# Performance work log

Measured on AMD Instinct MI355X. Metric: run time of the kernel, lower is better.

## Reference

```python
import jax, jax.numpy as jnp
import numpy as np

B, N, OBS_DIM = 64, 512, 128
HIDDEN_DIM, MESSAGE_DIM, ACTION_DIM = 256, 128, 16


def _dense_params(key, din, dout):
    kw, kb = jax.random.split(key)
    W = jax.random.normal(kw, (din, dout), jnp.float32) * 0.02
    b = jnp.zeros((dout,), jnp.float32)
    return W, b


def setup_inputs() -> dict:
    key = jax.random.key(0)
    ks = jax.random.split(key, 12)
    obs_batch = jax.random.normal(ks[0], (B, N, OBS_DIM), jnp.float32)
    dones_batch = jnp.zeros((B, N), jnp.bool_)
    We, be = _dense_params(ks[1], OBS_DIM, HIDDEN_DIM)
    Wc, bc = _dense_params(ks[2], HIDDEN_DIM, MESSAGE_DIM // 4)
    Wn, bn = _dense_params(ks[3], HIDDEN_DIM, MESSAGE_DIM // 2)
    Wb, bb = _dense_params(ks[4], HIDDEN_DIM, MESSAGE_DIM // 4)
    Wi, bi = _dense_params(ks[5], HIDDEN_DIM, 1)
    Wq, bq = _dense_params(ks[6], HIDDEN_DIM, MESSAGE_DIM)
    Wk, bk = _dense_params(ks[7], MESSAGE_DIM, MESSAGE_DIM)
    Wv, bv = _dense_params(ks[8], MESSAGE_DIM, MESSAGE_DIM)
    Wp, bp = _dense_params(ks[9], HIDDEN_DIM + MESSAGE_DIM, HIDDEN_DIM)
    Wa, ba = _dense_params(ks[10], HIDDEN_DIM, ACTION_DIM)
    Wcr, bcr = _dense_params(ks[11], HIDDEN_DIM, 1)
    return {"obs_batch": obs_batch, "dones_batch": dones_batch,
            "We": We, "be": be, "Wc": Wc, "bc": bc, "Wn": Wn, "bn": bn,
            "Wb": Wb, "bb": bb, "Wi": Wi, "bi": bi, "Wq": Wq, "bq": bq,
            "Wk": Wk, "bk": bk, "Wv": Wv, "bv": bv, "Wp": Wp, "bp": bp,
            "Wa": Wa, "ba": ba, "Wcr": Wcr, "bcr": bcr}


def reference(obs_batch, dones_batch, We, be, Wc, bc, Wn, bn, Wb, bb, Wi, bi,
              Wq, bq, Wk, bk, Wv, bv, Wp, bp, Wa, ba, Wcr, bcr):
    dense = lambda x, W, b: x @ W + b
    encoded = jax.nn.relu(dense(obs_batch, We, be))                 # [B,N,H]
    messages = jnp.concatenate([dense(encoded, Wc, bc),
                                dense(encoded, Wn, bn),
                                dense(encoded, Wb, bb)], axis=-1)   # [B,N,M]
    importance = jax.nn.sigmoid(dense(encoded, Wi, bi))             # [B,N,1]
    Q = dense(encoded, Wq, bq)
    K = dense(messages, Wk, bk)
    V = dense(messages, Wv, bv)
    scores = jnp.einsum('bqd,bkd->bqk', Q, K) / jnp.sqrt(jnp.float32(MESSAGE_DIM))
    importance_weights = importance * jnp.transpose(importance, (0, 2, 1))  # [B,N,N]
    scores = scores * importance_weights
    norms = jnp.linalg.norm(obs_batch, axis=-1, keepdims=True)      # [B,N,1]
    obs_sim = jnp.einsum('bid,bjd->bij', obs_batch, obs_batch)
    obs_sim = obs_sim / (norms + 1e-08)
    obs_sim = obs_sim / (jnp.transpose(norms, (0, 2, 1)) + 1e-08)
    scores = scores + obs_sim * 0.5
    attn = jax.nn.softmax(scores, axis=-1)
    aggregated = jnp.einsum('bqk,bkd->bqd', attn, V)                # [B,N,M]
    combined = jnp.concatenate([encoded, aggregated], axis=-1)
    x = jax.nn.relu(dense(combined, Wp, bp))
    logits = dense(x, Wa, ba)
    value = dense(x, Wcr, bcr).squeeze(-1)
    return (logits, value)
```

## Files before the change

### kernel.cpp

```cpp
#include <hip/hip_runtime.h>
#include <math.h>


typedef __attribute__((ext_vector_type(8))) short short8;
typedef __attribute__((ext_vector_type(4))) float f32x4;

#define RSQRT_D 0.08838834764831843f
#define MFMA __builtin_amdgcn_mfma_f32_16x16x32_bf16

__device__ __forceinline__ unsigned short f2bf(float f) {
  union { float f; unsigned u; } v; v.f = f;
  return (unsigned short)((v.u + 0x7FFFu + ((v.u >> 16) & 1u)) >> 16);
}
__device__ __forceinline__ float bf2f(unsigned short h) {
  union { unsigned u; float f; } v; v.u = ((unsigned)h) << 16;
  return v.f;
}
__device__ __forceinline__ unsigned pack2(float a, float b) {
  return (unsigned)f2bf(a) | ((unsigned)f2bf(b) << 16);
}
__device__ __forceinline__ short8 ld8(const unsigned short* p) {
  return *(const short8*)p;
}
__device__ __forceinline__ void gl16(const unsigned short* g,
                                     unsigned short* l) {
  __builtin_amdgcn_global_load_lds(
      (const __attribute__((address_space(1))) unsigned int*)(const void*)g,
      (__attribute__((address_space(3))) unsigned int*)(void*)l, 16, 0, 0);
}

__global__ __launch_bounds__(256) void prep_all(
    const float* __restrict__ obs, const float* __restrict__ We,
    const float* __restrict__ Wq, const float* __restrict__ Wk,
    const float* __restrict__ Wv, const float* __restrict__ Wp,
    const float* __restrict__ Wc, const float* __restrict__ Wn,
    const float* __restrict__ Wb, const float* __restrict__ bc,
    const float* __restrict__ bn, const float* __restrict__ bb,
    const float* __restrict__ Wa, const float* __restrict__ Wcr,
    const float* __restrict__ ba, const float* __restrict__ bcr,
    const float* __restrict__ bq, const float* __restrict__ bk,
    const float* __restrict__ bv, unsigned short* __restrict__ WeT,
    unsigned short* __restrict__ Wqkv, unsigned short* __restrict__ WpT,
    unsigned short* __restrict__ WaCrT, float* __restrict__ bqkv,
    unsigned short* __restrict__ obs_bf, unsigned short* __restrict__ As,
    unsigned short* __restrict__ Bs, float* __restrict__ logits,
    float* __restrict__ value) {
  const int bid = blockIdx.x, tid = threadIdx.x;
  if (bid < 673) {
    int idx = bid * 256 + tid;
    if (idx < 32768) {
      int n = idx >> 7, k = idx & 127;
      WeT[idx] = f2bf(We[k * 256 + n]);
    } else if (idx < 65536) {
      int i = idx - 32768;
      int n = i >> 8, k = i & 255;
      Wqkv[i] = f2bf(Wq[k * 128 + n]);
    } else if (idx < 163840) {
      int i = idx - 65536;
      int n = i / 384, k = i - n * 384;
      WpT[i] = f2bf(Wp[k * 256 + n]);
    } else if (idx < 172032) {
      int i = idx - 163840;
      int n = i >> 8, k = i & 255;
      float v = (n < 16) ? Wa[k * 16 + n] : (n == 16) ? Wcr[k] : 0.f;
      WaCrT[i] = f2bf(v);
    } else if (idx < 172160) {
      int i = idx - 172032;
      bqkv[i] = bq[i];
    }
  } else if (bid < 2721) {
    const int wave = tid >> 6, lane = tid & 63;
    const int t0 = (bid - 673) * 16 + wave * 4;
#pragma unroll
    for (int it = 0; it < 4; ++it) {
      int t = t0 + it;
      const float* row = obs + (size_t)t * 128;
      float2 o = *(const float2*)(row + lane * 2);
      float s2 = o.x * o.x + o.y * o.y;
#pragma unroll
      for (int off = 1; off < 64; off <<= 1) s2 += __shfl_xor(s2, off);
      float inv = 1.f / (sqrtf(s2) + 1e-8f);
      ((unsigned*)obs_bf)[(size_t)t * 64 + lane] = pack2(o.x, o.y);
      ((unsigned*)As)[(size_t)t * 128 + 64 + lane] =
          pack2(o.x * 0.5f * inv, o.y * 0.5f * inv);
      ((unsigned*)Bs)[(size_t)t * 128 + 64 + lane] =
          pack2(o.x * inv, o.y * inv);
    }
  } else if (bid < 4897) {
    int i = (bid - 2721) * 256 + tid;
    if (i < 524288) logits[i] = ba[i & 15];
    else value[i - 524288] = bcr[0];
  } else if (bid < 4905) {
    const int wb = bid - 4897;
    const int lane = tid & 63, wave = tid >> 6;
    const int quad = lane >> 4, l16 = lane & 15;
    const int r0 = wb * 32;
    f32x4 acc[2][4];
#pragma unroll
    for (int i = 0; i < 2; ++i)
#pragma unroll
      for (int j = 0; j < 4; ++j) acc[i][j] = (f32x4){0.f, 0.f, 0.f, 0.f};
#pragma unroll
    for (int kc = 0; kc < 4; ++kc) {
      short8 af[2], bf[4];
#pragma unroll
      for (int i = 0; i < 2; ++i) {
        int n = r0 + i * 16 + l16;
        const float* src = (n < 128) ? (Wk + n) : (Wv + (n - 128));
        short8 v;
#pragma unroll
        for (int e = 0; e < 8; ++e)
          v[e] = (short)f2bf(src[(size_t)(kc * 32 + quad * 8 + e) * 128]);
        af[i] = v;
      }
#pragma unroll
      for (int j = 0; j < 4; ++j) {
        int h = wave * 64 + j * 16 + l16;
        int m0 = kc * 32 + quad * 8;
        const float* p = (m0 < 32)   ? (Wc + (size_t)h * 32 + m0)
                       : (m0 < 96)   ? (Wn + (size_t)h * 64 + (m0 - 32))
                                     : (Wb + (size_t)h * 32 + (m0 - 96));
        short8 v;
#pragma unroll
        for (int e = 0; e < 8; ++e) v[e] = (short)f2bf(p[e]);
        bf[j] = v;
      }
#pragma unroll
      for (int i = 0; i < 2; ++i)
#pragma unroll
        for (int j = 0; j < 4; ++j)
          acc[i][j] = MFMA(af[i], bf[j], acc[i][j], 0, 0, 0);
    }
#pragma unroll
    for (int i = 0; i < 2; ++i) {
      const int row = r0 + i * 16 + quad * 4;
#pragma unroll
      for (int j = 0; j < 4; ++j) {
        const int col = wave * 64 + j * 16 + l16;
#pragma unroll
        for (int r = 0; r < 4; ++r)
          Wqkv[(size_t)(128 + row + r) * 256 + col] = f2bf(acc[i][j][r]);
      }
    }
  } else {
    int i = tid;
    float acc = (i < 128) ? bk[i] : bv[i - 128];
    for (int m = 0; m < 128; ++m) {
      float bmv = (m < 32) ? bc[m] : (m < 96) ? bn[m - 32] : bb[m - 96];
      float w = (i < 128) ? Wk[(size_t)m * 128 + i]
                          : Wv[(size_t)m * 128 + (i - 128)];
      acc += bmv * bf2f(f2bf(w));
    }
    bqkv[128 + i] = acc;
  }
}

__global__ __launch_bounds__(256, 2) void encqkv(
    const unsigned short* __restrict__ obs_bf,
    const unsigned short* __restrict__ WeT, const float* __restrict__ be,
    const float* __restrict__ Wi, const float* __restrict__ bi,
    const unsigned short* __restrict__ Wqkv, const float* __restrict__ bqkv,
    unsigned short* __restrict__ enc, unsigned short* __restrict__ As,
    unsigned short* __restrict__ Bs, unsigned short* __restrict__ vT) {
  __shared__ char smem[81920];
  unsigned short* Asr = (unsigned short*)smem;
  unsigned short* Bsr = (unsigned short*)(smem + 16384);
  unsigned short* encl = (unsigned short*)smem;
  unsigned short* Bq = (unsigned short*)(smem + 32768);
  float* imp_lds = (float*)(smem + 65536);
  const int tid = threadIdx.x, lane = tid & 63, wave = tid >> 6;
  const int quad = lane >> 4, l16 = lane & 15;
  const int bm0 = blockIdx.x * 64;

#pragma unroll
  for (int it = 0; it < 4; ++it) {
    int c = it * 256 + tid;
    int row = c >> 4, ch = c & 15;
    gl16(obs_bf + (size_t)(bm0 + row) * 128 + ((ch ^ (row & 15)) << 3),
         Asr + it * 2048 + wave * 512);
  }
#pragma unroll
  for (int it = 0; it < 16; ++it) {
    int c = it * 256 + tid;
    int row = c >> 4, ch = c & 15;
    gl16(WeT + (size_t)row * 128 + ((ch ^ (row & 15)) << 3),
         Bsr + it * 2048 + wave * 512);
  }
  __syncthreads();

  f32x4 acc[4][4];
#pragma unroll
  for (int i = 0; i < 4; ++i)
#pragma unroll
    for (int j = 0; j < 4; ++j) acc[i][j] = (f32x4){0.f, 0.f, 0.f, 0.f};
#pragma unroll
  for (int ks = 0; ks < 4; ++ks) {
    short8 af[4], bf[4];
#pragma unroll
    for (int mi = 0; mi < 4; ++mi) {
      int row = mi * 16 + l16;
      af[mi] = *(const short8*)&Asr[row * 128 + (((ks * 4 + quad) ^ (row & 15)) << 3)];
    }
#pragma unroll
    for (int ni = 0; ni < 4; ++ni) {
      int row = wave * 64 + ni * 16 + l16;
      bf[ni] = *(const short8*)&Bsr[row * 128 + (((ks * 4 + quad) ^ (row & 15)) << 3)];
    }
#pragma unroll
    for (int mi = 0; mi < 4; ++mi)
#pragma unroll
      for (int ni = 0; ni < 4; ++ni)
        acc[mi][ni] = MFMA(af[mi], bf[ni], acc[mi][ni], 0, 0, 0);
  }
  __syncthreads();

  if (tid < 64) imp_lds[tid] = 0.f;
  __syncthreads();

  {
#pragma unroll
    for (int i = 0; i < 4; ++i) {
      int row = i * 32 + (tid >> 3);
      gl16(Wqkv + (size_t)row * 256 + (((tid & 7) ^ (row & 7)) << 3),
           Bq + i * 2048 + wave * 512);
    }
  }

  const float bi0 = bi[0];
#pragma unroll
  for (int mi = 0; mi < 4; ++mi) {
    const int rowl = mi * 16 + quad * 4;
    float ip[4] = {0.f, 0.f, 0.f, 0.f};
#pragma unroll
    for (int ni = 0; ni < 4; ++ni) {
      const int col = wave * 64 + ni * 16 + l16;
      const float bvv = be[col], wv = Wi[col];
      const int kh = col >> 7, ic = col & 127;
#pragma unroll
      for (int r = 0; r < 4; ++r) {
        const int row = rowl + r;
        float v = fmaxf(acc[mi][ni][r] + bvv, 0.f);
        enc[(size_t)(bm0 + row) * 256 + col] = f2bf(v);
        encl[kh * 8192 + row * 128 + (((ic >> 3) ^ (row & 15)) << 3) + (ic & 7)] =
            f2bf(v);
        ip[r] += v * wv;
      }
    }
#pragma unroll
    for (int r = 0; r < 4; ++r) {
#pragma unroll
      for (int off = 1; off < 16; off <<= 1) ip[r] += __shfl_xor(ip[r], off);
    }
    if (l16 == 0) {
#pragma unroll
      for (int r = 0; r < 4; ++r) atomicAdd(&imp_lds[rowl + r], ip[r]);
    }
  }
  __syncthreads();

  const int wm = wave & 1, wn = wave >> 1;
  for (int ct = 0; ct < 3; ++ct) {
    f32x4 a2[2][4];
#pragma unroll
    for (int i = 0; i < 2; ++i)
#pragma unroll
      for (int j = 0; j < 4; ++j) a2[i][j] = (f32x4){0.f, 0.f, 0.f, 0.f};
#pragma unroll
    for (int kt = 0; kt < 4; ++kt) {
      if (kt < 3 || ct < 2) {
        const int nct = (kt < 3) ? ct : ct + 1;
        const int nkt = (kt < 3) ? kt + 1 : 0;
        const int nbo = ((kt + 1) & 1) * 8192;
#pragma unroll
        for (int i = 0; i < 4; ++i) {
          int row = i * 32 + (tid >> 3);
          gl16(Wqkv + (size_t)(nct * 128 + row) * 256 + nkt * 64 +
                   (((tid & 7) ^ (row & 7)) << 3),
               Bq + nbo + i * 2048 + wave * 512);
        }
      }
      const int bo = (kt & 1) * 8192;
#pragma unroll
      for (int ks2 = 0; ks2 < 2; ++ks2) {
        const int kc = kt * 2 + ks2;
        const int kh = kc >> 2, c4 = kc & 3;
        short8 af2[2], bf2[4];
#pragma unroll
        for (int mi = 0; mi < 2; ++mi) {
          int row = wm * 32 + mi * 16 + l16;
          af2[mi] = *(const short8*)&encl[kh * 8192 + row * 128 +
                                          (((c4 * 4 + quad) ^ (row & 15)) << 3)];
        }
#pragma unroll
        for (int ni = 0; ni < 4; ++ni) {
          int row = wn * 64 + ni * 16 + l16;
          bf2[ni] = *(const short8*)&Bq[bo + row * 64 +
                                        (((ks2 * 4 + quad) ^ (row & 7)) << 3)];
        }
#pragma unroll
        for (int mi = 0; mi < 2; ++mi)
#pragma unroll
          for (int ni = 0; ni < 4; ++ni)
            a2[mi][ni] = MFMA(af2[mi], bf2[ni], a2[mi][ni], 0, 0, 0);
      }
      __syncthreads();
    }

#pragma unroll
    for (int mi = 0; mi < 2; ++mi) {
      const int rowl = wm * 32 + mi * 16 + quad * 4;
      const int rowb = bm0 + rowl;
      float sg[4];
      if (ct < 2) {
        const float mult = (ct == 0) ? RSQRT_D : 1.0f;
#pragma unroll
        for (int r = 0; r < 4; ++r)
          sg[r] = mult / (1.f + __expf(-(imp_lds[rowl + r] + bi0)));
      }
#pragma unroll
      for (int ni = 0; ni < 4; ++ni) {
        const int col = wn * 64 + ni * 16 + l16;
        const float bvv = bqkv[ct * 128 + col];
        if (ct == 0) {
#pragma unroll
          for (int r = 0; r < 4; ++r)
            As[(size_t)(rowb + r) * 256 + col] =
                f2bf((a2[mi][ni][r] + bvv) * sg[r]);
        } else if (ct == 1) {
#pragma unroll
          for (int r = 0; r < 4; ++r)
            Bs[(size_t)(rowb + r) * 256 + col] =
                f2bf((a2[mi][ni][r] + bvv) * sg[r]);
        } else {
          uint2 o;
          o.x = pack2(a2[mi][ni][0] + bvv, a2[mi][ni][1] + bvv);
          o.y = pack2(a2[mi][ni][2] + bvv, a2[mi][ni][3] + bvv);
          *(uint2*)(vT + ((size_t)(rowb >> 9) * 128 + col) * 512 +
                    (rowb & 511)) = o;
        }
      }
    }
  }
}

__global__ __launch_bounds__(512, 4) void flash4b(
    const unsigned short* __restrict__ As, const unsigned short* __restrict__ Bs,
    const unsigned short* __restrict__ vT, unsigned short* __restrict__ agg) {
  __shared__ unsigned short Ub[16384];
  __shared__ unsigned short Pp[8192];
  __shared__ float redm[2][64];
  __shared__ float reds[2][64];
  const int tid = threadIdx.x, lane = tid & 63, wave = tid >> 6;
  const int quad = lane >> 4, l16 = lane & 15;
  const int wm = wave & 3, wn = wave >> 2;
  const int b = blockIdx.x & 63;
  const int qt = blockIdx.x >> 6;
  const size_t tok0 = (size_t)b * 512 + qt * 64;
  const int srow = tid >> 4, slc = tid & 15;
  const int qr8 = tid >> 3, ql8 = tid & 7;

  short8 af[8];
#pragma unroll
  for (int kc = 0; kc < 8; ++kc)
    af[kc] = ld8(As + (tok0 + wm * 16 + l16) * 256 + kc * 32 + quad * 8);

  f32x4 s[4][4];
#pragma unroll
  for (int kt = 0; kt < 4; ++kt)
#pragma unroll
    for (int nt = 0; nt < 4; ++nt) s[kt][nt] = (f32x4){0.f, 0.f, 0.f, 0.f};

  auto qstage = [&](int c) {
    const int kt_ = c >> 2, dq_ = c & 3;
#pragma unroll
    for (int r2 = 0; r2 < 2; ++r2) {
      int row = r2 * 64 + qr8;
      gl16(Bs + ((size_t)b * 512 + kt_ * 128 + row) * 256 + dq_ * 64 +
               ((ql8 ^ (row & 7)) << 3),
           Ub + (c & 1) * 8192 + r2 * 4096 + wave * 512);
    }
  };
  qstage(0);
  __syncthreads();
#pragma unroll 16
  for (int c = 0; c < 16; ++c) {
    if (c < 15) qstage(c + 1);
    const int kt = c >> 2, dq = c & 3;
    const int ub0 = (c & 1) * 8192;
#pragma unroll
    for (int kk2 = 0; kk2 < 2; ++kk2) {
      short8 bfr[4];
#pragma unroll
      for (int nt = 0; nt < 4; ++nt) {
        int rr = wn * 64 + nt * 16 + l16;
        bfr[nt] = *(const short8*)&Ub[ub0 + rr * 64 +
                                      (((kk2 * 2 + quad) ^ (rr & 7)) << 3)];
      }
#pragma unroll
      for (int nt = 0; nt < 4; ++nt)
        s[kt][nt] = MFMA(af[dq * 2 + kk2], bfr[nt], s[kt][nt], 0, 0, 0);
    }
    __syncthreads();
  }

  const int rbase = wm * 16 + quad * 4;
  float mt[4];
#pragma unroll
  for (int r = 0; r < 4; ++r) {
    float mv = -1e30f;
#pragma unroll
    for (int kt = 0; kt < 4; ++kt)
#pragma unroll
      for (int nt = 0; nt < 4; ++nt) mv = fmaxf(mv, s[kt][nt][r]);
#pragma unroll
    for (int off = 1; off < 16; off <<= 1) mv = fmaxf(mv, __shfl_xor(mv, off));
    mt[r] = mv;
  }
  if (l16 == 0) {
#pragma unroll
    for (int r = 0; r < 4; ++r) redm[wn][rbase + r] = mt[r];
  }
  __syncthreads();
  float lsum[4];
#pragma unroll
  for (int r = 0; r < 4; ++r) {
    float mfull = fmaxf(mt[r], redm[1 ^ wn][rbase + r]);
    float sum = 0.f;
#pragma unroll
    for (int kt = 0; kt < 4; ++kt)
#pragma unroll
      for (int nt = 0; nt < 4; ++nt) {
        float p = __expf(s[kt][nt][r] - mfull);
        s[kt][nt][r] = p;
        sum += p;
      }
#pragma unroll
    for (int off = 1; off < 16; off <<= 1) sum += __shfl_xor(sum, off);
    lsum[r] = sum;
  }
  if (l16 == 0) {
#pragma unroll
    for (int r = 0; r < 4; ++r) reds[wn][rbase + r] = lsum[r];
  }
  __syncthreads();
  float linv[4];
#pragma unroll
  for (int r = 0; r < 4; ++r)
    linv[r] = 1.0f / (lsum[r] + reds[1 ^ wn][rbase + r]);

  f32x4 oacc[4];
#pragma unroll
  for (int nt = 0; nt < 4; ++nt) oacc[nt] = (f32x4){0.f, 0.f, 0.f, 0.f};
#pragma unroll
  for (int vt = 0; vt < 4; ++vt) {
    __syncthreads();
#pragma unroll
    for (int nt = 0; nt < 4; ++nt) {
      const int col = wn * 64 + nt * 16 + l16;
#pragma unroll
      for (int r = 0; r < 4; ++r) {
        const int row = rbase + r;
        Pp[row * 128 + (((col >> 3) ^ (row & 15)) << 3) + (col & 7)] =
            f2bf(s[vt][nt][r]);
      }
    }
#pragma unroll
    for (int i = 0; i < 4; ++i) {
      int row = i * 32 + srow;
      gl16(vT + ((size_t)b * 128 + row) * 512 + vt * 128 +
               ((slc ^ (row & 15)) << 3),
           Ub + i * 4096 + wave * 512);
    }
    __syncthreads();
#pragma unroll
    for (int kk = 0; kk < 4; ++kk) {
      const int prow = wm * 16 + l16;
      short8 pa = *(const short8*)&Pp[prow * 128 + (((kk * 4 + quad) ^ (prow & 15)) << 3)];
#pragma unroll
      for (int nt = 0; nt < 4; ++nt) {
        int rr = wn * 64 + nt * 16 + l16;
        short8 vb = *(const short8*)&Ub[rr * 128 + (((kk * 4 + quad) ^ (rr & 15)) << 3)];
        oacc[nt] = MFMA(pa, vb, oacc[nt], 0, 0, 0);
      }
    }
  }
#pragma unroll
  for (int nt = 0; nt < 4; ++nt) {
    const int col = wn * 64 + nt * 16 + l16;
#pragma unroll
    for (int r = 0; r < 4; ++r)
      agg[(tok0 + rbase + r) * 128 + col] = f2bf(oacc[nt][r] * linv[r]);
  }
}

__global__ __launch_bounds__(256, 2) void xh_gemm(
    const unsigned short* __restrict__ enc, const unsigned short* __restrict__ agg,
    const unsigned short* __restrict__ WpT, const float* __restrict__ bp,
    const unsigned short* __restrict__ WaCrT, float* __restrict__ logits,
    float* __restrict__ value) {
  __shared__ unsigned short sm[16384];
  unsigned short* Asr = sm;
  unsigned short* Bsr = sm + 8192;
  const int tid = threadIdx.x, lane = tid & 63, wave = tid >> 6;
  const int quad = lane >> 4, l16 = lane & 15;
  const int wm = wave & 1, wn = wave >> 1;
  const int bm = blockIdx.y * 128, bn = blockIdx.x * 128;
  const int sr4 = tid >> 2, sl4 = tid & 3;

  f32x4 acc[4][4];
#pragma unroll
  for (int i = 0; i < 4; ++i)
#pragma unroll
    for (int j = 0; j < 4; ++j) acc[i][j] = (f32x4){0.f, 0.f, 0.f, 0.f};

  auto stage = [&](int t, int bo) {
    const unsigned short* Ap;
    int lda, kc;
    if (t < 8) { Ap = enc; lda = 256; kc = t * 32; }
    else       { Ap = agg; lda = 128; kc = t * 32 - 256; }
#pragma unroll
    for (int i = 0; i < 2; ++i) {
      int row = i * 64 + sr4;
      int sw = (sl4 ^ (row & 3)) << 3;
      gl16(Ap + (size_t)(bm + row) * lda + kc + sw,
           Asr + bo + i * 2048 + wave * 512);
      gl16(WpT + (size_t)(bn + row) * 384 + t * 32 + sw,
           Bsr + bo + i * 2048 + wave * 512);
    }
  };

  stage(0, 0);
  __syncthreads();
#pragma unroll 12
  for (int t = 0; t < 12; ++t) {
    if (t < 11) stage(t + 1, ((t + 1) & 1) * 4096);
    const int bo = (t & 1) * 4096;
    short8 af[4], bf[4];
#pragma unroll
    for (int mi = 0; mi < 4; ++mi) {
      int row = wm * 64 + mi * 16 + l16;
      af[mi] = *(const short8*)&Asr[bo + row * 32 + ((quad ^ (row & 3)) << 3)];
    }
#pragma unroll
    for (int ni = 0; ni < 4; ++ni) {
      int row = wn * 64 + ni * 16 + l16;
      bf[ni] = *(const short8*)&Bsr[bo + row * 32 + ((quad ^ (row & 3)) << 3)];
    }
#pragma unroll
    for (int mi = 0; mi < 4; ++mi)
#pragma unroll
      for (int ni = 0; ni < 4; ++ni)
        acc[mi][ni] = MFMA(af[mi], bf[ni], acc[mi][ni], 0, 0, 0);
    __syncthreads();
  }

#pragma unroll
  for (int mi = 0; mi < 4; ++mi) {
    const int row = wm * 64 + mi * 16 + quad * 4;
#pragma unroll
    for (int ni = 0; ni < 4; ++ni) {
      const int colc = wn * 64 + ni * 16 + l16;
      const float bv = bp[bn + colc];
#pragma unroll
      for (int r = 0; r < 4; ++r) {
        float v = fmaxf(acc[mi][ni][r] + bv, 0.f);
        sm[(row + r) * 128 + (((colc >> 3) ^ ((row + r) & 15)) << 3) + (colc & 7)] =
            f2bf(v);
      }
    }
  }
  __syncthreads();

  f32x4 h[2][2];
#pragma unroll
  for (int i = 0; i < 2; ++i)
#pragma unroll
    for (int j = 0; j < 2; ++j) h[i][j] = (f32x4){0.f, 0.f, 0.f, 0.f};
#pragma unroll
  for (int kc = 0; kc < 4; ++kc) {
    short8 xa[2], wb[2];
#pragma unroll
    for (int hm = 0; hm < 2; ++hm) {
      int row = wave * 32 + hm * 16 + l16;
      xa[hm] = *(const short8*)&sm[row * 128 + (((kc * 4 + quad) ^ (row & 15)) << 3)];
    }
#pragma unroll
    for (int hn = 0; hn < 2; ++hn)
      wb[hn] = ld8(WaCrT + (size_t)(hn * 16 + l16) * 256 + bn + kc * 32 + quad * 8);
#pragma unroll
    for (int hm = 0; hm < 2; ++hm)
#pragma unroll
      for (int hn = 0; hn < 2; ++hn)
        h[hm][hn] = MFMA(xa[hm], wb[hn], h[hm][hn], 0, 0, 0);
  }
#pragma unroll
  for (int hm = 0; hm < 2; ++hm) {
#pragma unroll
    for (int hn = 0; hn < 2; ++hn) {
      const int n = hn * 16 + l16;
#pragma unroll
      for (int r = 0; r < 4; ++r) {
        const int grow = bm + wave * 32 + hm * 16 + quad * 4 + r;
        if (n < 16)
          atomicAdd(&logits[(size_t)grow * 16 + n], h[hm][hn][r]);
        else if (n == 16)
          atomicAdd(&value[grow], h[hm][hn][r]);
      }
    }
  }
}

extern "C" void kernel_launch(void* const* d_in, const int* in_sizes, int n_in,
                              void* d_out, int out_size, void* d_ws,
                              size_t ws_size, hipStream_t stream) {
  const float* obs = (const float*)d_in[0];
  const float* We = (const float*)d_in[2];
  const float* be = (const float*)d_in[3];
  const float* Wc = (const float*)d_in[4];
  const float* bc = (const float*)d_in[5];
  const float* Wn = (const float*)d_in[6];
  const float* bn = (const float*)d_in[7];
  const float* Wb = (const float*)d_in[8];
  const float* bb = (const float*)d_in[9];
  const float* Wi = (const float*)d_in[10];
  const float* bi = (const float*)d_in[11];
  const float* Wq = (const float*)d_in[12];
  const float* bq = (const float*)d_in[13];
  const float* Wk = (const float*)d_in[14];
  const float* bk = (const float*)d_in[15];
  const float* Wv = (const float*)d_in[16];
  const float* bv = (const float*)d_in[17];
  const float* Wp = (const float*)d_in[18];
  const float* bp = (const float*)d_in[19];
  const float* Wa = (const float*)d_in[20];
  const float* ba = (const float*)d_in[21];
  const float* Wcr = (const float*)d_in[22];
  const float* bcr = (const float*)d_in[23];

  char* base = (char*)d_ws;
  unsigned short* enc_bf = (unsigned short*)(base);
  unsigned short* As     = (unsigned short*)(base + 16777216);
  unsigned short* Bs     = (unsigned short*)(base + 33554432);
  unsigned short* obsagg = (unsigned short*)(base + 50331648);
  unsigned short* vT     = (unsigned short*)(base + 58720256);
  unsigned short* WeT    = (unsigned short*)(base + 67239936);
  unsigned short* Wqkv   = (unsigned short*)(base + 67305472);
  unsigned short* WpT    = (unsigned short*)(base + 67633152);
  unsigned short* WaCrT  = (unsigned short*)(base + 67829760);
  float* bqkv            = (float*)(base + 67846656);

  float* logits = (float*)d_out;
  float* value = (float*)d_out + 524288;

  prep_all<<<4906, 256, 0, stream>>>(obs, We, Wq, Wk, Wv, Wp, Wc, Wn, Wb, bc,
                                     bn, bb, Wa, Wcr, ba, bcr, bq, bk, bv, WeT,
                                     Wqkv, WpT, WaCrT, bqkv, obsagg, As, Bs,
                                     logits, value);
  encqkv<<<512, 256, 0, stream>>>(obsagg, WeT, be, Wi, bi, Wqkv, bqkv, enc_bf,
                                  As, Bs, vT);
  flash4b<<<512, 512, 0, stream>>>(As, Bs, vT, obsagg);
  xh_gemm<<<dim3(2, 256), 256, 0, stream>>>(enc_bf, obsagg, WpT, bp, WaCrT,
                                            logits, value);
}
```

Measured before the change: 186.3 us.

## Retile final GEMM to full-width rows and drop output init and atomics

The projection GEMM now gives each block 64 rows by the full 256 output columns instead of 128x128 tiles. This lets the head GEMM (logits/value) run over the full hidden width inside one block and write outputs directly with the bias added. That removes the bias-initialization blocks from the prep kernel and all atomicAdd traffic on logits and value. In exchange each block reloads the whole WpT per k-step, uses twice the shared memory (64KB), and the head MFMA work is done by one 16-row slice per wave.

```diff
diff --git a/kernel.cpp b/kernel.cpp
--- a/kernel.cpp
+++ b/kernel.cpp
@@ -37,14 +37,12 @@
     const float* __restrict__ Wb, const float* __restrict__ bc,
     const float* __restrict__ bn, const float* __restrict__ bb,
     const float* __restrict__ Wa, const float* __restrict__ Wcr,
-    const float* __restrict__ ba, const float* __restrict__ bcr,
     const float* __restrict__ bq, const float* __restrict__ bk,
     const float* __restrict__ bv, unsigned short* __restrict__ WeT,
     unsigned short* __restrict__ Wqkv, unsigned short* __restrict__ WpT,
     unsigned short* __restrict__ WaCrT, float* __restrict__ bqkv,
     unsigned short* __restrict__ obs_bf, unsigned short* __restrict__ As,
-    unsigned short* __restrict__ Bs, float* __restrict__ logits,
-    float* __restrict__ value) {
+    unsigned short* __restrict__ Bs) {
   const int bid = blockIdx.x, tid = threadIdx.x;
   if (bid < 673) {
     int idx = bid * 256 + tid;
@@ -86,12 +84,8 @@
       ((unsigned*)Bs)[(size_t)t * 128 + 64 + lane] =
           pack2(o.x * inv, o.y * inv);
     }
-  } else if (bid < 4897) {
-    int i = (bid - 2721) * 256 + tid;
-    if (i < 524288) logits[i] = ba[i & 15];
-    else value[i - 524288] = bcr[0];
-  } else if (bid < 4905) {
-    const int wb = bid - 4897;
+  } else if (bid < 2729) {
+    const int wb = bid - 2721;
     const int lane = tid & 63, wave = tid >> 6;
     const int quad = lane >> 4, l16 = lane & 15;
     const int r0 = wb * 32;
@@ -496,15 +490,13 @@
 __global__ __launch_bounds__(256, 2) void xh_gemm(
     const unsigned short* __restrict__ enc, const unsigned short* __restrict__ agg,
     const unsigned short* __restrict__ WpT, const float* __restrict__ bp,
-    const unsigned short* __restrict__ WaCrT, float* __restrict__ logits,
+    const unsigned short* __restrict__ WaCrT, const float* __restrict__ ba,
+    const float* __restrict__ bcr, float* __restrict__ logits,
     float* __restrict__ value) {
-  __shared__ unsigned short sm[16384];
-  unsigned short* Asr = sm;
-  unsigned short* Bsr = sm + 8192;
+  __shared__ unsigned short sm[32768];
   const int tid = threadIdx.x, lane = tid & 63, wave = tid >> 6;
   const int quad = lane >> 4, l16 = lane & 15;
-  const int wm = wave & 1, wn = wave >> 1;
-  const int bm = blockIdx.y * 128, bn = blockIdx.x * 128;
+  const int bm = blockIdx.x * 64;
   const int sr4 = tid >> 2, sl4 = tid & 3;
 
   f32x4 acc[4][4];
@@ -513,19 +505,23 @@
 #pragma unroll
     for (int j = 0; j < 4; ++j) acc[i][j] = (f32x4){0.f, 0.f, 0.f, 0.f};
 
-  auto stage = [&](int t, int bo) {
+  auto stage = [&](int t, int half) {
     const unsigned short* Ap;
     int lda, kc;
     if (t < 8) { Ap = enc; lda = 256; kc = t * 32; }
     else       { Ap = agg; lda = 128; kc = t * 32 - 256; }
-#pragma unroll
-    for (int i = 0; i < 2; ++i) {
+    {
+      int row = sr4;
+      int sw = (sl4 ^ (row & 3)) << 3;
+      gl16(Ap + (size_t)(bm + row) * lda + kc + sw,
+           sm + half * 2048 + wave * 512);
+    }
+#pragma unroll
+    for (int i = 0; i < 4; ++i) {
       int row = i * 64 + sr4;
       int sw = (sl4 ^ (row & 3)) << 3;
-      gl16(Ap + (size_t)(bm + row) * lda + kc + sw,
-           Asr + bo + i * 2048 + wave * 512);
-      gl16(WpT + (size_t)(bn + row) * 384 + t * 32 + sw,
-           Bsr + bo + i * 2048 + wave * 512);
+      gl16(WpT + (size_t)row * 384 + t * 32 + sw,
+           sm + 4096 + half * 8192 + i * 2048 + wave * 512);
     }
   };
 
@@ -533,18 +529,18 @@
   __syncthreads();
 #pragma unroll 12
   for (int t = 0; t < 12; ++t) {
-    if (t < 11) stage(t + 1, ((t + 1) & 1) * 4096);
-    const int bo = (t & 1) * 4096;
+    if (t < 11) stage(t + 1, (t + 1) & 1);
+    const int abo = (t & 1) * 2048, bbo = 4096 + (t & 1) * 8192;
     short8 af[4], bf[4];
 #pragma unroll
     for (int mi = 0; mi < 4; ++mi) {
-      int row = wm * 64 + mi * 16 + l16;
-      af[mi] = *(const short8*)&Asr[bo + row * 32 + ((quad ^ (row & 3)) << 3)];
+      int row = mi * 16 + l16;
+      af[mi] = *(const short8*)&sm[abo + row * 32 + ((quad ^ (row & 3)) << 3)];
     }
 #pragma unroll
     for (int ni = 0; ni < 4; ++ni) {
-      int row = wn * 64 + ni * 16 + l16;
-      bf[ni] = *(const short8*)&Bsr[bo + row * 32 + ((quad ^ (row & 3)) << 3)];
+      int row = wave * 64 + ni * 16 + l16;
+      bf[ni] = *(const short8*)&sm[bbo + row * 32 + ((quad ^ (row & 3)) << 3)];
     }
 #pragma unroll
     for (int mi = 0; mi < 4; ++mi)
@@ -556,56 +552,48 @@
 
 #pragma unroll
   for (int mi = 0; mi < 4; ++mi) {
-    const int row = wm * 64 + mi * 16 + quad * 4;
+    const int row0 = mi * 16 + quad * 4;
 #pragma unroll
     for (int ni = 0; ni < 4; ++ni) {
-      const int colc = wn * 64 + ni * 16 + l16;
-      const float bv = bp[bn + colc];
+      const int colc = wave * 64 + ni * 16 + l16;
+      const float bv = bp[colc];
 #pragma unroll
       for (int r = 0; r < 4; ++r) {
+        const int row = row0 + r;
         float v = fmaxf(acc[mi][ni][r] + bv, 0.f);
-        sm[(row + r) * 128 + (((colc >> 3) ^ ((row + r) & 15)) << 3) + (colc & 7)] =
+        sm[row * 256 + ((((colc >> 3) ^ (row & 15))) << 3) + (colc & 7)] =
             f2bf(v);
       }
     }
   }
   __syncthreads();
 
-  f32x4 h[2][2];
-#pragma unroll
-  for (int i = 0; i < 2; ++i)
-#pragma unroll
-    for (int j = 0; j < 2; ++j) h[i][j] = (f32x4){0.f, 0.f, 0.f, 0.f};
-#pragma unroll
-  for (int kc = 0; kc < 4; ++kc) {
-    short8 xa[2], wb[2];
-#pragma unroll
-    for (int hm = 0; hm < 2; ++hm) {
-      int row = wave * 32 + hm * 16 + l16;
-      xa[hm] = *(const short8*)&sm[row * 128 + (((kc * 4 + quad) ^ (row & 15)) << 3)];
-    }
-#pragma unroll
-    for (int hn = 0; hn < 2; ++hn)
-      wb[hn] = ld8(WaCrT + (size_t)(hn * 16 + l16) * 256 + bn + kc * 32 + quad * 8);
-#pragma unroll
-    for (int hm = 0; hm < 2; ++hm)
-#pragma unroll
-      for (int hn = 0; hn < 2; ++hn)
-        h[hm][hn] = MFMA(xa[hm], wb[hn], h[hm][hn], 0, 0, 0);
-  }
-#pragma unroll
-  for (int hm = 0; hm < 2; ++hm) {
+  f32x4 h[2];
+#pragma unroll
+  for (int j = 0; j < 2; ++j) h[j] = (f32x4){0.f, 0.f, 0.f, 0.f};
+#pragma unroll
+  for (int kc = 0; kc < 8; ++kc) {
+    short8 xa;
+    {
+      int row = wave * 16 + l16;
+      xa = *(const short8*)&sm[row * 256 + (((kc * 4 + quad) ^ (row & 15)) << 3)];
+    }
 #pragma unroll
     for (int hn = 0; hn < 2; ++hn) {
-      const int n = hn * 16 + l16;
-#pragma unroll
-      for (int r = 0; r < 4; ++r) {
-        const int grow = bm + wave * 32 + hm * 16 + quad * 4 + r;
-        if (n < 16)
-          atomicAdd(&logits[(size_t)grow * 16 + n], h[hm][hn][r]);
-        else if (n == 16)
-          atomicAdd(&value[grow], h[hm][hn][r]);
-      }
+      short8 wb = ld8(WaCrT + (size_t)(hn * 16 + l16) * 256 + kc * 32 + quad * 8);
+      h[hn] = MFMA(xa, wb, h[hn], 0, 0, 0);
+    }
+  }
+#pragma unroll
+  for (int hn = 0; hn < 2; ++hn) {
+    const int n = hn * 16 + l16;
+#pragma unroll
+    for (int r = 0; r < 4; ++r) {
+      const int grow = bm + wave * 16 + quad * 4 + r;
+      if (n < 16)
+        logits[(size_t)grow * 16 + n] = ba[n] + h[hn][r];
+      else if (n == 16)
+        value[grow] = bcr[0] + h[hn][r];
     }
   }
 }
@@ -652,13 +640,12 @@
   float* logits = (float*)d_out;
   float* value = (float*)d_out + 524288;
 
-  prep_all<<<4906, 256, 0, stream>>>(obs, We, Wq, Wk, Wv, Wp, Wc, Wn, Wb, bc,
-                                     bn, bb, Wa, Wcr, ba, bcr, bq, bk, bv, WeT,
-                                     Wqkv, WpT, WaCrT, bqkv, obsagg, As, Bs,
-                                     logits, value);
+  prep_all<<<2730, 256, 0, stream>>>(obs, We, Wq, Wk, Wv, Wp, Wc, Wn, Wb, bc,
+                                     bn, bb, Wa, Wcr, bq, bk, bv, WeT, Wqkv,
+                                     WpT, WaCrT, bqkv, obsagg, As, Bs);
   encqkv<<<512, 256, 0, stream>>>(obsagg, WeT, be, Wi, bi, Wqkv, bqkv, enc_bf,
                                   As, Bs, vT);
   flash4b<<<512, 512, 0, stream>>>(As, Bs, vT, obsagg);
-  xh_gemm<<<dim3(2, 256), 256, 0, stream>>>(enc_bf, obsagg, WpT, bp, WaCrT,
-                                            logits, value);
-}
+  xh_gemm<<<512, 256, 0, stream>>>(enc_bf, obsagg, WpT, bp, WaCrT, ba, bcr,
+                                   logits, value);
+}
```

Result: no change. 185.7 us (-0.4%).
